# Performance work log

Measured on AMD Instinct MI355X. Metric: run time of the kernel, lower is better.

The kernel has to match this reference:

```python
import jax, jax.numpy as jnp
import numpy as np

C_EMB = 64  # n_embd


def setup_inputs() -> dict:
    key = jax.random.key(0)
    ks = jax.random.split(key, 7)
    B, T, C, H, BS = 2, 512, C_EMB, 64, 512
    s = lambda k, shp, sc: (jax.random.normal(k, shp, dtype=jnp.float32) * sc)
    return {
        "x": s(ks[0], (B, T, C), 1.0),
        "pos_table": s(ks[1], (BS, C), 0.02),
        "W1": s(ks[2], (C, 4 * C), (4 * C) ** -0.5),  # Linear(4C -> C), torch layout [out,in]
        "b1": s(ks[3], (C,), 0.01),
        "W2": s(ks[4], (1, C), C ** -0.5),            # Linear(C -> 1)
        "b2": s(ks[5], (1,), 0.01),
        "Wv": s(ks[6], (H, C), C ** -0.5),            # Linear(C -> H, bias=False)
    }


def reference(x, pos_table, W1, b1, W2, b2, Wv):
    B, T, C = x.shape
    # x1 = cat([pos_emb, x], -1): [B,T,2C]
    pos = pos_table[:T]  # [T,C]
    x1 = jnp.concatenate([jnp.broadcast_to(pos[None], (B, T, C)), x], axis=-1)  # [B,T,2C]
    # a2[b,i,j] = cat([x1[b,j], x1[b,i]]); Linear(4C->C) splits into key/query halves.
    Wk = W1[:, : 2 * C]   # acts on x1_j
    Wq = W1[:, 2 * C :]   # acts on x1_i
    hk = jnp.einsum('btd,cd->btc', x1, Wk)  # [B,T,C] indexed by j
    hq = jnp.einsum('btd,cd->btc', x1, Wq)  # [B,T,C] indexed by i
    hidden = jax.nn.relu(hq[:, :, None, :] + hk[:, None, :, :] + b1)  # [B,T(i),T(j),C]
    scores = jnp.einsum('bijc,c->bij', hidden, W2[0]) + b2[0]          # [B,T,T]
    wei = scores * (C ** -0.5)
    causal = jnp.tril(jnp.ones((T, T), dtype=bool))
    wei = jnp.where(causal[None], wei, -jnp.inf)
    wei = jax.nn.softmax(wei, axis=-1)  # dropout p=0 -> identity
    v = jnp.einsum('btc,hc->bth', x, Wv)  # [B,T,H]
    return jnp.einsum('bij,bjh->bih', wei, v)
```

## Files before the change

kernel.cpp:

```cpp
#include <hip/hip_runtime.h>
#include <math.h>

constexpr int TLEN = 512;
constexpr int CDIM = 64;
constexpr int BDIM = 2;

__global__ __launch_bounds__(256) void hk_kernel(
    const float* __restrict__ x, const float* __restrict__ pos,
    const float* __restrict__ W1, float4* __restrict__ hkt4)
{
    const int tid = threadIdx.x;
    const int r0g = blockIdx.x * 4;
    const int b   = r0g >> 9;
    const int t0  = r0g & (TLEN - 1);

    __shared__ float4 wk_s[64 * 32];
    __shared__ alignas(16) float x1s[4][128];
    __shared__ float hks[CDIM][5];

    const float4* W1f4 = (const float4*)W1;
    #pragma unroll
    for (int m = tid; m < 64 * 32; m += 256) {
        const int c = m >> 5, e4 = m & 31;
        wk_s[c * 32 + (e4 ^ (c & 31))] = W1f4[c * 64 + e4];
    }
    #pragma unroll
    for (int e = tid; e < 4 * 128; e += 256) {
        const int r4 = e >> 7, d = e & 127;
        const int grow = r0g + r4;
        const int tt = grow & (TLEN - 1);
        x1s[r4][d] = (d < CDIM) ? pos[tt * CDIM + d]
                                : x[grow * CDIM + (d - CDIM)];
    }
    __syncthreads();

    {
        const int sub = tid >> 6, c = tid & 63;
        const float4* xv = (const float4*)x1s[sub];
        const float4* wb = wk_s + c * 32;
        const int sw = c & 31;
        float4 a = make_float4(0.f, 0.f, 0.f, 0.f);
        #pragma unroll
        for (int d4 = 0; d4 < 32; ++d4) {
            const float4 xx = xv[d4];
            const float4 ww = wb[d4 ^ sw];
            a.x = fmaf(xx.x, ww.x, a.x); a.y = fmaf(xx.y, ww.y, a.y);
            a.z = fmaf(xx.z, ww.z, a.z); a.w = fmaf(xx.w, ww.w, a.w);
        }
        hks[c][sub] = (a.x + a.y) + (a.z + a.w);
    }
    __syncthreads();

    if (tid < 64) {
        const int c4 = tid >> 2, tl = tid & 3;
        const float4 v = make_float4(hks[c4 * 4 + 0][tl], hks[c4 * 4 + 1][tl],
                                     hks[c4 * 4 + 2][tl], hks[c4 * 4 + 3][tl]);
        hkt4[(b * 16 + c4) * TLEN + t0 + tl] = v;
    }
}

__global__ __launch_bounds__(512, 4) void attn_kernel(
    const float* __restrict__ x,  const float* __restrict__ pos,
    const float* __restrict__ W1, const float* __restrict__ b1,
    const float* __restrict__ W2, const float* __restrict__ b2,
    const float* __restrict__ Wv, const float4* __restrict__ hkt4,
    float* __restrict__ out)
{
    const int tid = threadIdx.x;
    const int idx = blockIdx.x;
    const int b   = idx & 1;
    const int p   = idx >> 1;
    int rr[2];
    rr[0] = p; rr[1] = (TLEN - 1) - p;

    __shared__ float4 wq_s[64 * 32];
    __shared__ float4 wv_s[64 * 16];
    __shared__ alignas(16) float x1s[2][128];
    __shared__ float hqp[2][CDIM][4];
    __shared__ alignas(16) float hq_sf[2][CDIM];
    __shared__ float4 w24_s[16];
    __shared__ alignas(16) float pS[2][TLEN];
    __shared__ float2 wredm[8];
    __shared__ float2 wreds[8];
    __shared__ float pvs[2][8][CDIM];
    __shared__ alignas(16) float o_s[2][CDIM];

    const float4* W1f4 = (const float4*)W1;
    #pragma unroll
    for (int m = tid; m < 64 * 32; m += 512) {
        const int c = m >> 5, e4 = m & 31;
        wq_s[c * 32 + (e4 ^ (c & 31))] = W1f4[c * 64 + 32 + e4];
    }
    const float4* Wvf4 = (const float4*)Wv;
    #pragma unroll
    for (int m = tid; m < 64 * 16; m += 512) {
        const int hh = m >> 4, e4 = m & 15;
        wv_s[hh * 16 + (e4 ^ (hh & 15))] = Wvf4[hh * 16 + e4];
    }
    if (tid < 256) {
        const int rp = tid >> 7, d = tid & 127;
        const int i  = rr[rp];
        x1s[rp][d] = (d < CDIM) ? pos[i * CDIM + d]
                                : x[(b * TLEN + i) * CDIM + (d - CDIM)];
    } else if (tid < 272) {
        w24_s[tid - 256] = ((const float4*)W2)[tid - 256];
    }
    __syncthreads();

    {
        const int k = tid >> 8, part = (tid >> 6) & 3, c = tid & 63;
        const float4* xv = ((const float4*)x1s[k]) + part * 8;
        const float4* wb = wq_s + c * 32;
        const int sw = c & 31;
        float4 a = make_float4(0.f, 0.f, 0.f, 0.f);
        #pragma unroll
        for (int d4 = 0; d4 < 8; ++d4) {
            const float4 xx = xv[d4];
            const float4 ww = wb[(part * 8 + d4) ^ sw];
            a.x = fmaf(xx.x, ww.x, a.x); a.y = fmaf(xx.y, ww.y, a.y);
            a.z = fmaf(xx.z, ww.z, a.z); a.w = fmaf(xx.w, ww.w, a.w);
        }
        hqp[k][c][part] = (a.x + a.y) + (a.z + a.w);
    }
    __syncthreads();
    if (tid < 128) {
        const int k = tid >> 6, c = tid & 63;
        hq_sf[k][c] = hqp[k][c][0] + hqp[k][c][1] + hqp[k][c][2]
                    + hqp[k][c][3] + b1[c];
    }
    __syncthreads();

    const float b2v = b2[0];
    const float4* hk4b = hkt4 + b * 16 * TLEN;
    const int j = tid;
    const int w = tid >> 6;

    float mw[2], pt[2], swv[2];
    #pragma unroll
    for (int k = 0; k < 2; ++k) {
        const int rk = rr[k];
        if ((w << 6) <= rk) {
            const float4* hq4 = (const float4*)hq_sf[k];
            float4 acc = make_float4(0.f, 0.f, 0.f, 0.f);
            #pragma unroll
            for (int c4 = 0; c4 < 16; ++c4) {
                const float4 kk = hk4b[c4 * TLEN + j];
                const float4 qq = hq4[c4];
                const float4 w2v = w24_s[c4];
                acc.x = fmaf(fmaxf(kk.x + qq.x, 0.f), w2v.x, acc.x);
                acc.y = fmaf(fmaxf(kk.y + qq.y, 0.f), w2v.y, acc.y);
                acc.z = fmaf(fmaxf(kk.z + qq.z, 0.f), w2v.z, acc.z);
                acc.w = fmaf(fmaxf(kk.w + qq.w, 0.f), w2v.w, acc.w);
            }
            const bool vld = (j <= rk);
            const float sv = vld ? ((acc.x + acc.y) + (acc.z + acc.w) + b2v)
                                   * 0.125f
                                 : -1e30f;
            float m = sv;
            #pragma unroll
            for (int off = 32; off > 0; off >>= 1)
                m = fmaxf(m, __shfl_xor(m, off));
            mw[k] = m;
            pt[k] = vld ? __expf(sv - m) : 0.f;
            float sm = pt[k];
            #pragma unroll
            for (int off = 32; off > 0; off >>= 1)
                sm += __shfl_xor(sm, off);
            swv[k] = sm;
        } else {
            mw[k] = -1e30f; pt[k] = 0.f; swv[k] = 0.f;
        }
    }
    if ((tid & 63) == 0) {
        wredm[w] = make_float2(mw[0], mw[1]);
        wreds[w] = make_float2(swv[0], swv[1]);
    }
    __syncthreads();

    float gm0 = -1e30f, gm1 = -1e30f;
    #pragma unroll
    for (int ww = 0; ww < 8; ++ww) {
        const float2 rm = wredm[ww];
        gm0 = fmaxf(gm0, rm.x);
        gm1 = fmaxf(gm1, rm.y);
    }
    float gs0 = 0.f, gs1 = 0.f;
    #pragma unroll
    for (int ww = 0; ww < 8; ++ww) {
        const float2 rm = wredm[ww];
        const float2 rs = wreds[ww];
        gs0 = fmaf(rs.x, __expf(rm.x - gm0), gs0);
        gs1 = fmaf(rs.y, __expf(rm.y - gm1), gs1);
    }
    pS[0][j] = pt[0] * (__expf(mw[0] - gm0) / gs0);
    pS[1][j] = pt[1] * (__expf(mw[1] - gm1) / gs1);
    __syncthreads();

    const int h = tid & 63;
    const int g = w;
    const float* xh = x + b * TLEN * CDIM + h;
    const int nj4 = (rr[1] >> 2) + 1;
    float4 a0 = make_float4(0.f, 0.f, 0.f, 0.f);
    float4 a1 = a0;
    for (int j4 = g; j4 < nj4; j4 += 8) {
        const int j0 = j4 * 4;
        const float4 p1v = ((const float4*)pS[1])[j4];
        const float x0 = xh[j0 * CDIM];
        const float x1 = xh[(j0 + 1) * CDIM];
        const float x2 = xh[(j0 + 2) * CDIM];
        const float x3 = xh[(j0 + 3) * CDIM];
        a1.x = fmaf(p1v.x, x0, a1.x); a1.y = fmaf(p1v.y, x1, a1.y);
        a1.z = fmaf(p1v.z, x2, a1.z); a1.w = fmaf(p1v.w, x3, a1.w);
        if (j0 <= rr[0]) {
            const float4 p0v = ((const float4*)pS[0])[j4];
            a0.x = fmaf(p0v.x, x0, a0.x); a0.y = fmaf(p0v.y, x1, a0.y);
            a0.z = fmaf(p0v.z, x2, a0.z); a0.w = fmaf(p0v.w, x3, a0.w);
        }
    }
    pvs[0][g][h] = (a0.x + a0.y) + (a0.z + a0.w);
    pvs[1][g][h] = (a1.x + a1.y) + (a1.z + a1.w);
    __syncthreads();
    if (tid < 128) {
        const int k = tid >> 6, hh = tid & 63;
        float o = pvs[k][0][hh];
        #pragma unroll
        for (int ww = 1; ww < 8; ++ww) o += pvs[k][ww][hh];
        o_s[k][hh] = o;
    }
    __syncthreads();
    if (tid < 128) {
        const int k = tid >> 6, hh = tid & 63;
        const float4* wb = wv_s + hh * 16;
        const int sw = hh & 15;
        const float4* o4 = (const float4*)o_s[k];
        float4 a = make_float4(0.f, 0.f, 0.f, 0.f);
        #pragma unroll
        for (int c4 = 0; c4 < 16; ++c4) {
            const float4 wwv = wb[c4 ^ sw];
            const float4 oo = o4[c4];
            a.x = fmaf(oo.x, wwv.x, a.x); a.y = fmaf(oo.y, wwv.y, a.y);
            a.z = fmaf(oo.z, wwv.z, a.z); a.w = fmaf(oo.w, wwv.w, a.w);
        }
        out[(b * TLEN + rr[k]) * CDIM + hh] = (a.x + a.y) + (a.z + a.w);
    }
}

extern "C" void kernel_launch(void* const* d_in, const int* in_sizes, int n_in,
                              void* d_out, int out_size, void* d_ws, size_t ws_size,
                              hipStream_t stream)
{
    const float* x   = (const float*)d_in[0];
    const float* pos = (const float*)d_in[1];
    const float* W1  = (const float*)d_in[2];
    const float* b1  = (const float*)d_in[3];
    const float* W2  = (const float*)d_in[4];
    const float* b2  = (const float*)d_in[5];
    const float* Wv  = (const float*)d_in[6];
    float* out = (float*)d_out;

    float4* hkt4 = (float4*)d_ws;

    hk_kernel<<<BDIM * TLEN / 4, 256, 0, stream>>>(x, pos, W1, hkt4);
    attn_kernel<<<BDIM * TLEN / 2, 512, 0, stream>>>(x, pos, W1, b1, W2, b2, Wv,
                                                     hkt4, out);
}
```

Before: 20.46 us.

## Process four query rows per block with 1024 threads to amortize weight staging

The attention kernel now handles four query rows per block instead of two, using 1024 threads split into two halves. Each half pairs a short causal row with a long one to balance work. The block count is halved, so the per-block shared-memory loads of Wq and Wv are spread across twice as many rows, cutting redundant global weight traffic. In exchange blocks are larger and use more LDS, which lowers the number of resident blocks and the scheduling flexibility per CU.

```diff
diff --git a/kernel.cpp b/kernel.cpp
--- a/kernel.cpp
+++ b/kernel.cpp
@@ -59,52 +59,61 @@
     }
 }
 
-__global__ __launch_bounds__(512, 4) void attn_kernel(
+__global__ __launch_bounds__(1024, 4) void attn_kernel(
     const float* __restrict__ x,  const float* __restrict__ pos,
     const float* __restrict__ W1, const float* __restrict__ b1,
     const float* __restrict__ W2, const float* __restrict__ b2,
     const float* __restrict__ Wv, const float4* __restrict__ hkt4,
     float* __restrict__ out)
 {
-    const int tid = threadIdx.x;
-    const int idx = blockIdx.x;
-    const int b   = idx & 1;
-    const int p   = idx >> 1;
-    int rr[2];
-    rr[0] = p; rr[1] = (TLEN - 1) - p;
+    const int tid  = threadIdx.x;
+    const int idx  = blockIdx.x;
+    const int b    = idx & 1;
+    const int p    = idx >> 1;
+    int r[4];
+    r[0] = p; r[1] = p + 128; r[2] = 383 - p; r[3] = 511 - p;
+
+    const int half = tid >> 9;
+    const int jj   = tid & 511;
+    const int gw   = (tid >> 6) & 7;
+    const int wg   = tid >> 6;
+    const int ka   = half ? 1 : 2;
+    const int kb   = half ? 2 : 3;
+    const int kA   = half ? 1 : 0;
+    const int kB   = half ? 2 : 3;
 
     __shared__ float4 wq_s[64 * 32];
     __shared__ float4 wv_s[64 * 16];
-    __shared__ alignas(16) float x1s[2][128];
-    __shared__ float hqp[2][CDIM][4];
-    __shared__ alignas(16) float hq_sf[2][CDIM];
+    __shared__ alignas(16) float x1s[4][128];
+    __shared__ float hqp[4][CDIM][4];
+    __shared__ alignas(16) float hq_sf[4][CDIM];
     __shared__ float4 w24_s[16];
-    __shared__ alignas(16) float pS[2][TLEN];
-    __shared__ float2 wredm[8];
-    __shared__ float2 wreds[8];
-    __shared__ float pvs[2][8][CDIM];
-    __shared__ alignas(16) float o_s[2][CDIM];
+    __shared__ alignas(16) float pS[4][TLEN];
+    __shared__ float2 wredm[16];
+    __shared__ float2 wreds[16];
+    __shared__ float pvs[4][8][CDIM];
+    __shared__ alignas(16) float o_s[4][CDIM];
 
     const float4* W1f4 = (const float4*)W1;
     #pragma unroll
-    for (int m = tid; m < 64 * 32; m += 512) {
+    for (int m = tid; m < 64 * 32; m += 1024) {
         const int c = m >> 5, e4 = m & 31;
         wq_s[c * 32 + (e4 ^ (c & 31))] = W1f4[c * 64 + 32 + e4];
     }
-    const float4* Wvf4 = (const float4*)Wv;
-    #pragma unroll
-    for (int m = tid; m < 64 * 16; m += 512) {
-        const int hh = m >> 4, e4 = m & 15;
-        wv_s[hh * 16 + (e4 ^ (hh & 15))] = Wvf4[hh * 16 + e4];
-    }
-    if (tid < 256) {
+    {
+        const int m = tid & 1023;
+        if (m < 64 * 16) {
+            const int hh = m >> 4, e4 = m & 15;
+            wv_s[hh * 16 + (e4 ^ (hh & 15))] = ((const float4*)Wv)[hh * 16 + e4];
+        }
+    }
+    if (tid < 512) {
         const int rp = tid >> 7, d = tid & 127;
-        const int i  = rr[rp];
+        const int i  = r[rp];
         x1s[rp][d] = (d < CDIM) ? pos[i * CDIM + d]
                                 : x[(b * TLEN + i) * CDIM + (d - CDIM)];
-    } else if (tid < 272) {
-        w24_s[tid - 256] = ((const float4*)W2)[tid - 256];
-    }
+    }
+    if (tid >= 512 && tid < 528) w24_s[tid - 512] = ((const float4*)W2)[tid - 512];
     __syncthreads();
 
     {
@@ -123,7 +132,7 @@
         hqp[k][c][part] = (a.x + a.y) + (a.z + a.w);
     }
     __syncthreads();
-    if (tid < 128) {
+    if (tid < 256) {
         const int k = tid >> 6, c = tid & 63;
         hq_sf[k][c] = hqp[k][c][0] + hqp[k][c][1] + hqp[k][c][2]
                     + hqp[k][c][3] + b1[c];
@@ -132,19 +141,19 @@
 
     const float b2v = b2[0];
     const float4* hk4b = hkt4 + b * 16 * TLEN;
-    const int j = tid;
-    const int w = tid >> 6;
-
-    float mw[2], pt[2], swv[2];
-    #pragma unroll
-    for (int k = 0; k < 2; ++k) {
-        const int rk = rr[k];
-        if ((w << 6) <= rk) {
-            const float4* hq4 = (const float4*)hq_sf[k];
+    const int wbase = gw << 6;
+
+    float mw2[2], pt2[2], sw2[2];
+    const int myk[2] = { kA, kB };
+    #pragma unroll
+    for (int q = 0; q < 2; ++q) {
+        const int rk = r[myk[q]];
+        if (wbase <= rk) {
+            const float4* hq4 = (const float4*)hq_sf[myk[q]];
             float4 acc = make_float4(0.f, 0.f, 0.f, 0.f);
             #pragma unroll
             for (int c4 = 0; c4 < 16; ++c4) {
-                const float4 kk = hk4b[c4 * TLEN + j];
+                const float4 kk = hk4b[c4 * TLEN + jj];
                 const float4 qq = hq4[c4];
                 const float4 w2v = w24_s[c4];
                 acc.x = fmaf(fmaxf(kk.x + qq.x, 0.f), w2v.x, acc.x);
@@ -152,7 +161,7 @@
                 acc.z = fmaf(fmaxf(kk.z + qq.z, 0.f), w2v.z, acc.z);
                 acc.w = fmaf(fmaxf(kk.w + qq.w, 0.f), w2v.w, acc.w);
             }
-            const bool vld = (j <= rk);
+            const bool vld = (jj <= rk);
             const float sv = vld ? ((acc.x + acc.y) + (acc.z + acc.w) + b2v)
                                    * 0.125f
                                  : -1e30f;
@@ -160,67 +169,70 @@
             #pragma unroll
             for (int off = 32; off > 0; off >>= 1)
                 m = fmaxf(m, __shfl_xor(m, off));
-            mw[k] = m;
-            pt[k] = vld ? __expf(sv - m) : 0.f;
-            float sm = pt[k];
+            mw2[q] = m;
+            pt2[q] = vld ? __expf(sv - m) : 0.f;
+            float sm = pt2[q];
             #pragma unroll
             for (int off = 32; off > 0; off >>= 1)
                 sm += __shfl_xor(sm, off);
-            swv[k] = sm;
+            sw2[q] = sm;
         } else {
-            mw[k] = -1e30f; pt[k] = 0.f; swv[k] = 0.f;
+            mw2[q] = -1e30f; pt2[q] = 0.f; sw2[q] = 0.f;
         }
     }
     if ((tid & 63) == 0) {
-        wredm[w] = make_float2(mw[0], mw[1]);
-        wreds[w] = make_float2(swv[0], swv[1]);
-    }
-    __syncthreads();
-
-    float gm0 = -1e30f, gm1 = -1e30f;
-    #pragma unroll
-    for (int ww = 0; ww < 8; ++ww) {
-        const float2 rm = wredm[ww];
-        gm0 = fmaxf(gm0, rm.x);
-        gm1 = fmaxf(gm1, rm.y);
-    }
-    float gs0 = 0.f, gs1 = 0.f;
-    #pragma unroll
-    for (int ww = 0; ww < 8; ++ww) {
-        const float2 rm = wredm[ww];
-        const float2 rs = wreds[ww];
-        gs0 = fmaf(rs.x, __expf(rm.x - gm0), gs0);
-        gs1 = fmaf(rs.y, __expf(rm.y - gm1), gs1);
-    }
-    pS[0][j] = pt[0] * (__expf(mw[0] - gm0) / gs0);
-    pS[1][j] = pt[1] * (__expf(mw[1] - gm1) / gs1);
+        wredm[wg] = make_float2(mw2[0], mw2[1]);
+        wreds[wg] = make_float2(sw2[0], sw2[1]);
+    }
+    __syncthreads();
+
+    {
+        const int base = half * 8;
+        float gmA = -1e30f, gmB = -1e30f;
+        #pragma unroll
+        for (int ww = 0; ww < 8; ++ww) {
+            const float2 rm = wredm[base + ww];
+            gmA = fmaxf(gmA, rm.x);
+            gmB = fmaxf(gmB, rm.y);
+        }
+        float gsA = 0.f, gsB = 0.f;
+        #pragma unroll
+        for (int ww = 0; ww < 8; ++ww) {
+            const float2 rm = wredm[base + ww];
+            const float2 rs = wreds[base + ww];
+            gsA = fmaf(rs.x, __expf(rm.x - gmA), gsA);
+            gsB = fmaf(rs.y, __expf(rm.y - gmB), gsB);
+        }
+        pS[kA][jj] = pt2[0] * (__expf(mw2[0] - gmA) / gsA);
+        pS[kB][jj] = pt2[1] * (__expf(mw2[1] - gmB) / gsB);
+    }
     __syncthreads();
 
     const int h = tid & 63;
-    const int g = w;
     const float* xh = x + b * TLEN * CDIM + h;
-    const int nj4 = (rr[1] >> 2) + 1;
-    float4 a0 = make_float4(0.f, 0.f, 0.f, 0.f);
-    float4 a1 = a0;
-    for (int j4 = g; j4 < nj4; j4 += 8) {
+    const int rkA = r[kA], rkB = r[kB];
+    const int nj4 = (rkB >> 2) + 1;
+    float4 aA = make_float4(0.f, 0.f, 0.f, 0.f);
+    float4 aB = aA;
+    for (int j4 = gw; j4 < nj4; j4 += 8) {
         const int j0 = j4 * 4;
-        const float4 p1v = ((const float4*)pS[1])[j4];
+        const float4 pB4 = ((const float4*)pS[kB])[j4];
         const float x0 = xh[j0 * CDIM];
         const float x1 = xh[(j0 + 1) * CDIM];
         const float x2 = xh[(j0 + 2) * CDIM];
         const float x3 = xh[(j0 + 3) * CDIM];
-        a1.x = fmaf(p1v.x, x0, a1.x); a1.y = fmaf(p1v.y, x1, a1.y);
-        a1.z = fmaf(p1v.z, x2, a1.z); a1.w = fmaf(p1v.w, x3, a1.w);
-        if (j0 <= rr[0]) {
-            const float4 p0v = ((const float4*)pS[0])[j4];
-            a0.x = fmaf(p0v.x, x0, a0.x); a0.y = fmaf(p0v.y, x1, a0.y);
-            a0.z = fmaf(p0v.z, x2, a0.z); a0.w = fmaf(p0v.w, x3, a0.w);
-        }
-    }
-    pvs[0][g][h] = (a0.x + a0.y) + (a0.z + a0.w);
-    pvs[1][g][h] = (a1.x + a1.y) + (a1.z + a1.w);
-    __syncthreads();
-    if (tid < 128) {
+        aB.x = fmaf(pB4.x, x0, aB.x); aB.y = fmaf(pB4.y, x1, aB.y);
+        aB.z = fmaf(pB4.z, x2, aB.z); aB.w = fmaf(pB4.w, x3, aB.w);
+        if (j0 <= rkA) {
+            const float4 pA4 = ((const float4*)pS[kA])[j4];
+            aA.x = fmaf(pA4.x, x0, aA.x); aA.y = fmaf(pA4.y, x1, aA.y);
+            aA.z = fmaf(pA4.z, x2, aA.z); aA.w = fmaf(pA4.w, x3, aA.w);
+        }
+    }
+    pvs[kA][gw][h] = (aA.x + aA.y) + (aA.z + aA.w);
+    pvs[kB][gw][h] = (aB.x + aB.y) + (aB.z + aB.w);
+    __syncthreads();
+    if (tid < 256) {
         const int k = tid >> 6, hh = tid & 63;
         float o = pvs[k][0][hh];
         #pragma unroll
@@ -228,7 +240,7 @@
         o_s[k][hh] = o;
     }
     __syncthreads();
-    if (tid < 128) {
+    if (tid < 256) {
         const int k = tid >> 6, hh = tid & 63;
         const float4* wb = wv_s + hh * 16;
         const int sw = hh & 15;
@@ -241,7 +253,7 @@
             a.x = fmaf(oo.x, wwv.x, a.x); a.y = fmaf(oo.y, wwv.y, a.y);
             a.z = fmaf(oo.z, wwv.z, a.z); a.w = fmaf(oo.w, wwv.w, a.w);
         }
-        out[(b * TLEN + rr[k]) * CDIM + hh] = (a.x + a.y) + (a.z + a.w);
+        out[(b * TLEN + r[k]) * CDIM + hh] = (a.x + a.y) + (a.z + a.w);
     }
 }
 
@@ -261,6 +273,6 @@
     float4* hkt4 = (float4*)d_ws;
 
     hk_kernel<<<BDIM * TLEN / 4, 256, 0, stream>>>(x, pos, W1, hkt4);
-    attn_kernel<<<BDIM * TLEN / 2, 512, 0, stream>>>(x, pos, W1, b1, W2, b2, Wv,
-                                                     hkt4, out);
+    attn_kernel<<<BDIM * TLEN / 4, 1024, 0, stream>>>(x, pos, W1, b1, W2, b2, Wv,
+                                                      hkt4, out);
 }
```

Result: slower. 20.88 us (+2.0%).
